# Kernel optimization log

Measured on AMD Instinct MI355X. Metric: run time of the kernel, lower is better.

The kernel has to match this reference:

```python
import jax, jax.numpy as jnp
import numpy as np

NEG_INF = -jnp.inf

def setup_inputs() -> dict:
    key = jax.random.key(0)
    k1, k2, k3, k4, k5 = jax.random.split(key, 5)
    b, n, d = 8, 1024, 2048
    s = 1.0 / np.sqrt(d)  # keep activations well-scaled (kaiming-ish)
    return {
        "y":  jax.random.normal(k1, (b, n, d), dtype=jnp.float32),
        "Wk": jax.random.normal(k2, (d, d), dtype=jnp.float32) * s,
        "Wq": jax.random.normal(k3, (d, d), dtype=jnp.float32) * s,
        "Wv": jax.random.normal(k4, (d, d), dtype=jnp.float32) * s,
        "Wo": jax.random.normal(k5, (d, d), dtype=jnp.float32) * s,
    }

def reference(y, Wk, Wq, Wv, Wo):
    # nn.Linear(bias=False): x @ W.T
    K = jnp.einsum('bnd,ed->bne', y, Wk)
    Q = 0.1 * jnp.einsum('bnd,ed->bne', y, Wq)
    V = jnp.einsum('bnd,ed->bne', y, Wv)
    # logits[b,i,j] = Q_i . K_j
    logits = jnp.einsum('bid,bjd->bij', Q, K)
    n = y.shape[1]
    diag = jnp.eye(n, dtype=bool)  # self-exclusion mask on the diagonal
    logits = jnp.where(diag[None, :, :], NEG_INF, logits)
    # NOTE: softmax over dim=1 (rows of the score matrix), non-standard axis
    attention_weights = jax.nn.softmax(logits, axis=1)
    # dropout(p=0.5) treated as identity (eval/deterministic reference)
    # torch: (V^T @ W)^T  ==  out[b,i,:] = sum_j W[b,j,i] * V[b,j,:]
    out = jnp.einsum('bji,bjd->bid', attention_weights, V)
    out = jnp.einsum('bid,ed->bie', out, Wo)
    return (out, attention_weights)
```

## Files before the change

kernel.cpp:

```cpp
#include <hip/hip_runtime.h>

typedef unsigned short u16;
typedef __attribute__((ext_vector_type(8))) __bf16 bf16x8;
typedef __attribute__((ext_vector_type(4))) float f32x4;
typedef __attribute__((ext_vector_type(4))) unsigned short u16x4;
typedef __attribute__((ext_vector_type(8))) unsigned short u16x8;

#define GLOBAL_AS __attribute__((address_space(1)))
#define LDS_AS __attribute__((address_space(3)))

__device__ __forceinline__ void gload_lds16(const void* g, void* l) {
    __builtin_amdgcn_global_load_lds((const GLOBAL_AS void*)g, (LDS_AS void*)l, 16, 0, 0);
}

__device__ __forceinline__ u16 f2bf(float f) {
    union { float f; unsigned u; } x; x.f = f;
    unsigned r = x.u + 0x7FFFu + ((x.u >> 16) & 1u);
    return (u16)(r >> 16);
}
__device__ __forceinline__ float bf2f(u16 h) {
    union { unsigned u; float f; } x; x.u = ((unsigned)h) << 16;
    return x.f;
}
struct BfPair { u16 h, l; };
__device__ __forceinline__ BfPair split2(float v) {
    BfPair p;
    p.h = f2bf(v);
    p.l = f2bf(v - bf2f(p.h));
    return p;
}

#define TM 128
#define TN 128
#define BK 64

__global__ __launch_bounds__(256) void conv_bf(
    const float* __restrict__ src, u16* __restrict__ dst, int n8)
{
    const int stride = gridDim.x * 256;
    for (int i = blockIdx.x * 256 + threadIdx.x; i < n8; i += stride) {
        const float* g = src + (size_t)i * 8;
        f32x4 v0 = *(const f32x4*)g;
        f32x4 v1 = *(const f32x4*)(g + 4);
        u16x8 w;
        #pragma unroll
        for (int e = 0; e < 4; ++e) { w[e] = f2bf(v0[e]); w[e + 4] = f2bf(v1[e]); }
        *(u16x8*)(dst + (size_t)i * 8) = w;
    }
}

__global__ __launch_bounds__(256) void transpose3(
    const float* __restrict__ s0, const float* __restrict__ s1, const float* __restrict__ s2,
    u16* __restrict__ d0, u16* __restrict__ d1, u16* __restrict__ d2)
{
    __shared__ float tile[64][65];
    const int z = blockIdx.z;
    const float* S = (z == 0) ? s0 : (z == 1) ? s1 : s2;
    u16* D = (z == 0) ? d0 : (z == 1) ? d1 : d2;
    const int x0 = blockIdx.x * 64;
    const int y0 = blockIdx.y * 64;
    const int t = threadIdx.x;
    const int rt = t >> 4;
    const int c4 = (t & 15) * 4;

    #pragma unroll
    for (int p = 0; p < 4; ++p) {
        const int r = p * 16 + rt;
        f32x4 v = *(const f32x4*)(S + (size_t)(y0 + r) * 2048 + x0 + c4);
        #pragma unroll
        for (int e = 0; e < 4; ++e) tile[r][c4 + e] = v[e];
    }
    __syncthreads();
    #pragma unroll
    for (int p = 0; p < 4; ++p) {
        const int a = p * 16 + rt;
        u16x4 w;
        #pragma unroll
        for (int e = 0; e < 4; ++e) w[e] = f2bf(tile[c4 + e][a]);
        *(u16x4*)(D + (size_t)(x0 + a) * 2048 + y0 + c4) = w;
    }
}

__global__ __launch_bounds__(256, 2) void gemm_pre(
    const u16* __restrict__ A0, const u16* __restrict__ B0,
    u16* __restrict__ GH, u16* __restrict__ GL, float alpha0,
    const u16* __restrict__ A1, const u16* __restrict__ B1, u16* __restrict__ U1,
    int N, int K)
{
    __shared__ u16 As0[TM * BK];
    __shared__ u16 Bs0[TN * BK];
    __shared__ u16 As1[TM * BK];
    __shared__ u16 Bs1[TN * BK];

    const int n0 = blockIdx.x * TN;
    const int m0 = blockIdx.y * TM;
    const int tid = threadIdx.x;
    const int lane = tid & 63;
    const int wave = tid >> 6;
    const int wm = (wave >> 1) * 64;
    const int wn = (wave & 1) * 64;
    const int quad = lane >> 4;
    const int lrow = lane & 15;

    f32x4 acc0[4][4] = {};
    f32x4 acc1[4][4] = {};

    for (int k0 = 0; k0 < K; k0 += BK) {
        #pragma unroll
        for (int r = 0; r < 4; ++r) {
            const int wbase = r * 4096 + wave * 1024;
            const int o = wbase + lane * 16;
            const int row = o >> 7;
            const int ce = (o & 127) >> 1;
            const size_t ao = (size_t)(m0 + row) * K + k0 + ce;
            const size_t bo = (size_t)(n0 + row) * K + k0 + ce;
            gload_lds16(A0 + ao, (char*)As0 + wbase);
            gload_lds16(B0 + bo, (char*)Bs0 + wbase);
            gload_lds16(A1 + ao, (char*)As1 + wbase);
            gload_lds16(B1 + bo, (char*)Bs1 + wbase);
        }
        __syncthreads();

        #pragma unroll
        for (int kk = 0; kk < BK; kk += 32) {
            bf16x8 a0[4], b0[4], a1[4], b1[4];
            #pragma unroll
            for (int t = 0; t < 4; ++t) {
                const int ra = (wm + t * 16 + lrow) * BK + kk + quad * 8;
                const int rb = (wn + t * 16 + lrow) * BK + kk + quad * 8;
                a0[t] = *(const bf16x8*)&As0[ra];
                b0[t] = *(const bf16x8*)&Bs0[rb];
                a1[t] = *(const bf16x8*)&As1[ra];
                b1[t] = *(const bf16x8*)&Bs1[rb];
            }
            #pragma unroll
            for (int ti = 0; ti < 4; ++ti)
                #pragma unroll
                for (int tj = 0; tj < 4; ++tj) {
                    acc0[ti][tj] = __builtin_amdgcn_mfma_f32_16x16x32_bf16(
                        a0[ti], b0[tj], acc0[ti][tj], 0, 0, 0);
                    acc1[ti][tj] = __builtin_amdgcn_mfma_f32_16x16x32_bf16(
                        a1[ti], b1[tj], acc1[ti][tj], 0, 0, 0);
                }
        }
        __syncthreads();
    }

    #pragma unroll
    for (int ti = 0; ti < 4; ++ti)
        #pragma unroll
        for (int tj = 0; tj < 4; ++tj) {
            const int nn = n0 + wn + tj * 16 + lrow;
            #pragma unroll
            for (int r2 = 0; r2 < 4; ++r2) {
                const int mm = m0 + wm + ti * 16 + quad * 4 + r2;
                BfPair p = split2(acc0[ti][tj][r2] * alpha0);
                GH[(size_t)mm * N + nn] = p.h;
                GL[(size_t)mm * N + nn] = p.l;
                U1[(size_t)mm * N + nn] = f2bf(acc1[ti][tj][r2]);
            }
        }
}

template <bool OSPLIT>
__global__ __launch_bounds__(256) void gemm_bs(
    const u16* __restrict__ A,
    const u16* __restrict__ Bh, const u16* __restrict__ Bl,
    void* __restrict__ C, void* __restrict__ C2,
    int M, int N, int K, size_t sAb, size_t sBb, size_t sCb)
{
    __shared__ u16 As[TM * BK];
    __shared__ u16 Bsh[TN * BK];
    __shared__ u16 Bsl[TN * BK];

    const int z = blockIdx.z;
    const u16* Ab  = (const u16*)((const char*)A + (size_t)z * sAb);
    const u16* Bhb = (const u16*)((const char*)Bh + (size_t)z * sBb);
    const u16* Blb = (const u16*)((const char*)Bl + (size_t)z * sBb);

    const int n0 = blockIdx.x * TN;
    const int m0 = blockIdx.y * TM;
    const int tid = threadIdx.x;
    const int lane = tid & 63;
    const int wave = tid >> 6;
    const int wm = (wave >> 1) * 64;
    const int wn = (wave & 1) * 64;
    const int quad = lane >> 4;
    const int lrow = lane & 15;

    f32x4 acc[4][4] = {};

    for (int k0 = 0; k0 < K; k0 += BK) {
        #pragma unroll
        for (int r = 0; r < 4; ++r) {
            const int wbase = r * 4096 + wave * 1024;
            const int o = wbase + lane * 16;
            const int row = o >> 7;
            const int ce = (o & 127) >> 1;
            const size_t ao = (size_t)(m0 + row) * K + k0 + ce;
            const size_t bo = (size_t)(n0 + row) * K + k0 + ce;
            gload_lds16(Ab + ao, (char*)As + wbase);
            gload_lds16(Bhb + bo, (char*)Bsh + wbase);
            gload_lds16(Blb + bo, (char*)Bsl + wbase);
        }
        __syncthreads();

        #pragma unroll
        for (int kk = 0; kk < BK; kk += 32) {
            bf16x8 af[4], bh[4], bl[4];
            #pragma unroll
            for (int t = 0; t < 4; ++t) {
                const int ra = (wm + t * 16 + lrow) * BK + kk + quad * 8;
                const int rb = (wn + t * 16 + lrow) * BK + kk + quad * 8;
                af[t] = *(const bf16x8*)&As[ra];
                bh[t] = *(const bf16x8*)&Bsh[rb];
                bl[t] = *(const bf16x8*)&Bsl[rb];
            }
            #pragma unroll
            for (int ti = 0; ti < 4; ++ti)
                #pragma unroll
                for (int tj = 0; tj < 4; ++tj) {
                    acc[ti][tj] = __builtin_amdgcn_mfma_f32_16x16x32_bf16(
                        af[ti], bl[tj], acc[ti][tj], 0, 0, 0);
                    acc[ti][tj] = __builtin_amdgcn_mfma_f32_16x16x32_bf16(
                        af[ti], bh[tj], acc[ti][tj], 0, 0, 0);
                }
        }
        __syncthreads();
    }

    if (OSPLIT) {
        u16* Chb = (u16*)((char*)C + (size_t)z * sCb);
        u16* Clb = (u16*)((char*)C2 + (size_t)z * sCb);
        #pragma unroll
        for (int ti = 0; ti < 4; ++ti)
            #pragma unroll
            for (int tj = 0; tj < 4; ++tj) {
                const int nn = n0 + wn + tj * 16 + lrow;
                #pragma unroll
                for (int r2 = 0; r2 < 4; ++r2) {
                    const int mm = m0 + wm + ti * 16 + quad * 4 + r2;
                    BfPair p = split2(acc[ti][tj][r2]);
                    Chb[(size_t)mm * N + nn] = p.h;
                    Clb[(size_t)mm * N + nn] = p.l;
                }
            }
    } else {
        float* Cb = (float*)((char*)C + (size_t)z * sCb);
        #pragma unroll
        for (int ti = 0; ti < 4; ++ti)
            #pragma unroll
            for (int tj = 0; tj < 4; ++tj) {
                const int nn = n0 + wn + tj * 16 + lrow;
                #pragma unroll
                for (int r2 = 0; r2 < 4; ++r2) {
                    const int mm = m0 + wm + ti * 16 + quad * 4 + r2;
                    Cb[(size_t)mm * N + nn] = acc[ti][tj][r2];
                }
            }
    }
}

__global__ __launch_bounds__(256, 2) void gemm_vo(
    const u16* __restrict__ A, const u16* __restrict__ B,
    u16* __restrict__ C,
    int M, int N, int K, size_t sBb, size_t sCb)
{
    __shared__ u16 As[TM * BK];
    __shared__ u16 Bs0[TN * BK];
    __shared__ u16 Bs1[TN * BK];

    const int z0 = blockIdx.z * 2;
    const u16* B0b = (const u16*)((const char*)B + (size_t)z0 * sBb);
    const u16* B1b = (const u16*)((const char*)B + (size_t)(z0 + 1) * sBb);

    const int n0 = blockIdx.x * TN;
    const int m0 = blockIdx.y * TM;
    const int tid = threadIdx.x;
    const int lane = tid & 63;
    const int wave = tid >> 6;
    const int wm = (wave >> 1) * 64;
    const int wn = (wave & 1) * 64;
    const int quad = lane >> 4;
    const int lrow = lane & 15;

    f32x4 acc0[4][4] = {};
    f32x4 acc1[4][4] = {};

    for (int k0 = 0; k0 < K; k0 += BK) {
        #pragma unroll
        for (int r = 0; r < 4; ++r) {
            const int wbase = r * 4096 + wave * 1024;
            const int o = wbase + lane * 16;
            const int row = o >> 7;
            const int ce = (o & 127) >> 1;
            const size_t ao = (size_t)(m0 + row) * K + k0 + ce;
            const size_t bo = (size_t)(n0 + row) * K + k0 + ce;
            gload_lds16(A + ao, (char*)As + wbase);
            gload_lds16(B0b + bo, (char*)Bs0 + wbase);
            gload_lds16(B1b + bo, (char*)Bs1 + wbase);
        }
        __syncthreads();

        #pragma unroll
        for (int kk = 0; kk < BK; kk += 32) {
            bf16x8 af[4], b0[4], b1[4];
            #pragma unroll
            for (int t = 0; t < 4; ++t) {
                const int ra = (wm + t * 16 + lrow) * BK + kk + quad * 8;
                const int rb = (wn + t * 16 + lrow) * BK + kk + quad * 8;
                af[t] = *(const bf16x8*)&As[ra];
                b0[t] = *(const bf16x8*)&Bs0[rb];
                b1[t] = *(const bf16x8*)&Bs1[rb];
            }
            #pragma unroll
            for (int ti = 0; ti < 4; ++ti)
                #pragma unroll
                for (int tj = 0; tj < 4; ++tj) {
                    acc0[ti][tj] = __builtin_amdgcn_mfma_f32_16x16x32_bf16(
                        af[ti], b0[tj], acc0[ti][tj], 0, 0, 0);
                    acc1[ti][tj] = __builtin_amdgcn_mfma_f32_16x16x32_bf16(
                        af[ti], b1[tj], acc1[ti][tj], 0, 0, 0);
                }
        }
        __syncthreads();
    }

    u16* C0 = (u16*)((char*)C + (size_t)z0 * sCb);
    u16* C1 = (u16*)((char*)C + (size_t)(z0 + 1) * sCb);
    #pragma unroll
    for (int ti = 0; ti < 4; ++ti)
        #pragma unroll
        for (int tj = 0; tj < 4; ++tj) {
            const int nn = n0 + wn + tj * 16 + lrow;
            #pragma unroll
            for (int r2 = 0; r2 < 4; ++r2) {
                const int mm = m0 + wm + ti * 16 + quad * 4 + r2;
                C0[(size_t)mm * N + nn] = f2bf(acc0[ti][tj][r2]);
                C1[(size_t)mm * N + nn] = f2bf(acc1[ti][tj][r2]);
            }
        }
}

__global__ __launch_bounds__(256) void gemm_fin(
    const u16* __restrict__ Ah, const u16* __restrict__ Al,
    const u16* __restrict__ B, float* __restrict__ C,
    int M, int N, int K, size_t sAb, size_t sBb, size_t sCb)
{
    __shared__ u16 Ash[TM * BK];
    __shared__ u16 Asl[TM * BK];
    __shared__ u16 Bs[TN * BK];

    const int z = blockIdx.z;
    const u16* Ahb = (const u16*)((const char*)Ah + (size_t)z * sAb);
    const u16* Alb = (const u16*)((const char*)Al + (size_t)z * sAb);
    const u16* Bb  = (const u16*)((const char*)B + (size_t)z * sBb);

    const int n0 = blockIdx.x * TN;
    const int m0 = blockIdx.y * TM;
    const int tid = threadIdx.x;
    const int lane = tid & 63;
    const int wave = tid >> 6;
    const int wm = (wave >> 1) * 64;
    const int wn = (wave & 1) * 64;
    const int quad = lane >> 4;
    const int lrow = lane & 15;

    f32x4 acc[4][4] = {};

    for (int k0 = 0; k0 < K; k0 += BK) {
        #pragma unroll
        for (int r = 0; r < 4; ++r) {
            const int wbase = r * 4096 + wave * 1024;
            const int o = wbase + lane * 16;
            const int row = o >> 7;
            const int ce = (o & 127) >> 1;
            const size_t ao = (size_t)(m0 + row) * K + k0 + ce;
            const size_t bo = (size_t)(n0 + row) * K + k0 + ce;
            gload_lds16(Ahb + ao, (char*)Ash + wbase);
            gload_lds16(Alb + ao, (char*)Asl + wbase);
            gload_lds16(Bb + bo, (char*)Bs + wbase);
        }
        __syncthreads();

        #pragma unroll
        for (int kk = 0; kk < BK; kk += 32) {
            bf16x8 ah[4], al[4], bfr[4];
            #pragma unroll
            for (int t = 0; t < 4; ++t) {
                const int ra = (wm + t * 16 + lrow) * BK + kk + quad * 8;
                ah[t] = *(const bf16x8*)&Ash[ra];
                al[t] = *(const bf16x8*)&Asl[ra];
                bfr[t] = *(const bf16x8*)&Bs[(wn + t * 16 + lrow) * BK + kk + quad * 8];
            }
            #pragma unroll
            for (int ti = 0; ti < 4; ++ti)
                #pragma unroll
                for (int tj = 0; tj < 4; ++tj) {
                    acc[ti][tj] = __builtin_amdgcn_mfma_f32_16x16x32_bf16(
                        al[ti], bfr[tj], acc[ti][tj], 0, 0, 0);
                    acc[ti][tj] = __builtin_amdgcn_mfma_f32_16x16x32_bf16(
                        ah[ti], bfr[tj], acc[ti][tj], 0, 0, 0);
                }
        }
        __syncthreads();
    }

    float* Cb = (float*)((char*)C + (size_t)z * sCb);
    #pragma unroll
    for (int ti = 0; ti < 4; ++ti)
        #pragma unroll
        for (int tj = 0; tj < 4; ++tj) {
            const int nn = n0 + wn + tj * 16 + lrow;
            #pragma unroll
            for (int r2 = 0; r2 < 4; ++r2) {
                const int mm = m0 + wm + ti * 16 + quad * 4 + r2;
                Cb[(size_t)mm * N + nn] = acc[ti][tj][r2];
            }
        }
}

__global__ __launch_bounds__(256) void softmax_split(
    const float* __restrict__ Lh, u16* __restrict__ Th, u16* __restrict__ Tl)
{
    const int lane = threadIdx.x & 63;
    const int wave = threadIdx.x >> 6;
    const size_t row = (size_t)blockIdx.x * 4 + wave;
    const int i = (int)(row & 1023);
    const float* src = Lh + row * 1024;
    const float NEG = -__builtin_inff();

    float v[16];
    float mx = NEG;
    #pragma unroll
    for (int cc = 0; cc < 4; ++cc) {
        f32x4 x = *(const f32x4*)(src + cc * 256 + lane * 4);
        #pragma unroll
        for (int e = 0; e < 4; ++e) {
            const int j = cc * 256 + lane * 4 + e;
            const float val = (j == i) ? NEG : x[e];
            v[cc * 4 + e] = val;
            mx = fmaxf(mx, val);
        }
    }
    #pragma unroll
    for (int off = 32; off > 0; off >>= 1) mx = fmaxf(mx, __shfl_xor(mx, off, 64));
    float s = 0.f;
    #pragma unroll
    for (int k = 0; k < 16; ++k) { v[k] = __expf(v[k] - mx); s += v[k]; }
    #pragma unroll
    for (int off = 32; off > 0; off >>= 1) s += __shfl_xor(s, off, 64);
    const float inv = 1.0f / s;

    #pragma unroll
    for (int cc = 0; cc < 4; ++cc) {
        u16x4 wh, wl;
        #pragma unroll
        for (int e = 0; e < 4; ++e) {
            BfPair p = split2(v[cc * 4 + e] * inv);
            wh[e] = p.h;
            wl[e] = p.l;
        }
        *(u16x4*)(Th + row * 1024 + cc * 256 + lane * 4) = wh;
        *(u16x4*)(Tl + row * 1024 + cc * 256 + lane * 4) = wl;
    }
}

__global__ __launch_bounds__(256) void transpose_attn_f32(
    const u16* __restrict__ Th, const u16* __restrict__ Tl, float* __restrict__ A)
{
    __shared__ float tile[64][65];
    const int bz = blockIdx.z;
    const int x0 = blockIdx.x * 64;
    const int y0 = blockIdx.y * 64;
    const size_t base = (size_t)bz * 1024 * 1024;
    float* dst = A + base;
    const int t = threadIdx.x;
    const int rt = t >> 4;
    const int c4 = (t & 15) * 4;

    #pragma unroll
    for (int p = 0; p < 4; ++p) {
        const int r = p * 16 + rt;
        const size_t off = base + (size_t)(y0 + r) * 1024 + x0 + c4;
        u16x4 vh = *(const u16x4*)(Th + off);
        u16x4 vl = *(const u16x4*)(Tl + off);
        #pragma unroll
        for (int e = 0; e < 4; ++e) tile[r][c4 + e] = bf2f(vh[e]) + bf2f(vl[e]);
    }
    __syncthreads();
    #pragma unroll
    for (int p = 0; p < 4; ++p) {
        const int a = p * 16 + rt;
        f32x4 w;
        #pragma unroll
        for (int e = 0; e < 4; ++e) w[e] = tile[c4 + e][a];
        *(f32x4*)(dst + (size_t)(x0 + a) * 1024 + y0 + c4) = w;
    }
}

extern "C" void kernel_launch(void* const* d_in, const int* in_sizes, int n_in,
                              void* d_out, int out_size, void* d_ws, size_t ws_size,
                              hipStream_t stream) {
    const float* y  = (const float*)d_in[0];
    const float* Wk = (const float*)d_in[1];
    const float* Wq = (const float*)d_in[2];
    const float* Wv = (const float*)d_in[3];
    const float* Wo = (const float*)d_in[4];

    const int b = 8, n = 1024, d = 2048;
    const int MB = b * n;
    const size_t MiB = 1024 * 1024;

    char* ws = (char*)d_ws;
    u16* yB  = (u16*)(ws);
    u16* WkT = (u16*)(ws + 32 * MiB);
    u16* WqT = (u16*)(ws + 40 * MiB);
    u16* WvT = (u16*)(ws + 48 * MiB);
    u16* WoB = (u16*)(ws + 56 * MiB);
    u16* GtH = (u16*)(ws + 64 * MiB);
    u16* GtL = (u16*)(ws + 72 * MiB);
    u16* UtB = (u16*)(ws + 80 * MiB);
    u16* ZcH = (u16*)(ws + 32 * MiB);
    u16* ZcL = (u16*)(ws + 88 * MiB);
    u16* Th  = (u16*)(ws + 32 * MiB);
    u16* Tl  = (u16*)(ws + 48 * MiB);
    u16* VOt = (u16*)(ws + 88 * MiB);

    float* outF = (float*)d_out;
    float* attF = outF + (size_t)MB * d;
    float* Lh   = (float*)d_out;

    dim3 blk(256);
    conv_bf<<<dim3(2048), blk, 0, stream>>>(y,  yB,  (MB * d) / 8);
    conv_bf<<<dim3(512),  blk, 0, stream>>>(Wo, WoB, (d * d) / 8);
    transpose3<<<dim3(32, 32, 3), blk, 0, stream>>>(Wk, Wq, Wv, WkT, WqT, WvT);
    gemm_pre<<<dim3(d / TN, d / TM, 1), blk, 0, stream>>>(
        WkT, WqT, GtH, GtL, 0.1f, WoB, WvT, UtB, d, d);
    gemm_bs<true><<<dim3(d / TN, MB / TM, 1), blk, 0, stream>>>(
        yB, GtH, GtL, ZcH, ZcL, MB, d, d, 0, 0, 0);
    gemm_bs<false><<<dim3(n / TN, n / TM, b), blk, 0, stream>>>(
        yB, ZcH, ZcL, Lh, nullptr, n, n, d,
        (size_t)n * d * 2, (size_t)n * d * 2, (size_t)n * n * 4);
    softmax_split<<<dim3(MB / 4), blk, 0, stream>>>(Lh, Th, Tl);
    transpose_attn_f32<<<dim3(16, 16, b), blk, 0, stream>>>(Th, Tl, attF);
    gemm_vo<<<dim3(n / TN, d / TM, b / 2), blk, 0, stream>>>(
        UtB, yB, VOt, d, n, d, (size_t)n * d * 2, (size_t)d * n * 2);
    gemm_fin<<<dim3(d / TN, n / TM, b), blk, 0, stream>>>(
        Th, Tl, VOt, outF, n, d, n,
        (size_t)n * n * 2, (size_t)d * n * 2, (size_t)n * d * 4);
}
```

Measured before the change: 643.8 us.

## Fuse logits and V·Wo GEMMs into one heterogeneous launch

Merges the batched logits GEMM (y·Zc split hi/lo) and the V·Wo GEMM into a single kernel whose first 512 blocks compute logits and remaining 1024 compute VOt, so both independent workloads fill the GPU together. It also drops the paired-batch register-heavy gemm_vo variant in favour of one batch per block. VOt is relocated into the output buffer's attention region, and the attention transpose is moved after gemm_fin so it runs once VOt is consumed. This removes one launch and a tail-effect gap, at the cost of a buffer-aliasing ordering dependency.

```diff
diff --git a/kernel.cpp b/kernel.cpp
--- a/kernel.cpp
+++ b/kernel.cpp
@@ -261,21 +261,15 @@
     }
 }
 
-__global__ __launch_bounds__(256, 2) void gemm_vo(
-    const u16* __restrict__ A, const u16* __restrict__ B,
-    u16* __restrict__ C,
-    int M, int N, int K, size_t sBb, size_t sCb)
-{
-    __shared__ u16 As[TM * BK];
-    __shared__ u16 Bs0[TN * BK];
-    __shared__ u16 Bs1[TN * BK];
-
-    const int z0 = blockIdx.z * 2;
-    const u16* B0b = (const u16*)((const char*)B + (size_t)z0 * sBb);
-    const u16* B1b = (const u16*)((const char*)B + (size_t)(z0 + 1) * sBb);
-
-    const int n0 = blockIdx.x * TN;
-    const int m0 = blockIdx.y * TM;
+__global__ __launch_bounds__(256) void gemm_lv(
+    const u16* __restrict__ yB, const u16* __restrict__ ZcH, const u16* __restrict__ ZcL,
+    float* __restrict__ Lh, const u16* __restrict__ Ut, u16* __restrict__ VOt)
+{
+    __shared__ u16 S0[TM * BK];
+    __shared__ u16 S1[TN * BK];
+    __shared__ u16 S2[TN * BK];
+
+    const int bid = blockIdx.x;
     const int tid = threadIdx.x;
     const int lane = tid & 63;
     const int wave = tid >> 6;
@@ -283,63 +277,115 @@
     const int wn = (wave & 1) * 64;
     const int quad = lane >> 4;
     const int lrow = lane & 15;
-
-    f32x4 acc0[4][4] = {};
-    f32x4 acc1[4][4] = {};
-
-    for (int k0 = 0; k0 < K; k0 += BK) {
-        #pragma unroll
-        for (int r = 0; r < 4; ++r) {
-            const int wbase = r * 4096 + wave * 1024;
-            const int o = wbase + lane * 16;
-            const int row = o >> 7;
-            const int ce = (o & 127) >> 1;
-            const size_t ao = (size_t)(m0 + row) * K + k0 + ce;
-            const size_t bo = (size_t)(n0 + row) * K + k0 + ce;
-            gload_lds16(A + ao, (char*)As + wbase);
-            gload_lds16(B0b + bo, (char*)Bs0 + wbase);
-            gload_lds16(B1b + bo, (char*)Bs1 + wbase);
-        }
-        __syncthreads();
-
-        #pragma unroll
-        for (int kk = 0; kk < BK; kk += 32) {
-            bf16x8 af[4], b0[4], b1[4];
-            #pragma unroll
-            for (int t = 0; t < 4; ++t) {
-                const int ra = (wm + t * 16 + lrow) * BK + kk + quad * 8;
-                const int rb = (wn + t * 16 + lrow) * BK + kk + quad * 8;
-                af[t] = *(const bf16x8*)&As[ra];
-                b0[t] = *(const bf16x8*)&Bs0[rb];
-                b1[t] = *(const bf16x8*)&Bs1[rb];
-            }
-            #pragma unroll
-            for (int ti = 0; ti < 4; ++ti)
-                #pragma unroll
-                for (int tj = 0; tj < 4; ++tj) {
-                    acc0[ti][tj] = __builtin_amdgcn_mfma_f32_16x16x32_bf16(
-                        af[ti], b0[tj], acc0[ti][tj], 0, 0, 0);
-                    acc1[ti][tj] = __builtin_amdgcn_mfma_f32_16x16x32_bf16(
-                        af[ti], b1[tj], acc1[ti][tj], 0, 0, 0);
-                }
-        }
-        __syncthreads();
-    }
-
-    u16* C0 = (u16*)((char*)C + (size_t)z0 * sCb);
-    u16* C1 = (u16*)((char*)C + (size_t)(z0 + 1) * sCb);
-    #pragma unroll
-    for (int ti = 0; ti < 4; ++ti)
-        #pragma unroll
-        for (int tj = 0; tj < 4; ++tj) {
-            const int nn = n0 + wn + tj * 16 + lrow;
-            #pragma unroll
-            for (int r2 = 0; r2 < 4; ++r2) {
-                const int mm = m0 + wm + ti * 16 + quad * 4 + r2;
-                C0[(size_t)mm * N + nn] = f2bf(acc0[ti][tj][r2]);
-                C1[(size_t)mm * N + nn] = f2bf(acc1[ti][tj][r2]);
-            }
-        }
+    const int K = 2048;
+
+    if (bid < 512) {
+        const int z = bid >> 6;
+        const int m0 = ((bid >> 3) & 7) * TM;
+        const int n0 = (bid & 7) * TN;
+        const u16* Ab  = yB  + (size_t)z * 1024 * 2048;
+        const u16* Bhb = ZcH + (size_t)z * 1024 * 2048;
+        const u16* Blb = ZcL + (size_t)z * 1024 * 2048;
+
+        f32x4 acc[4][4] = {};
+        for (int k0 = 0; k0 < K; k0 += BK) {
+            #pragma unroll
+            for (int r = 0; r < 4; ++r) {
+                const int wbase = r * 4096 + wave * 1024;
+                const int o = wbase + lane * 16;
+                const int row = o >> 7;
+                const int ce = (o & 127) >> 1;
+                const size_t ao = (size_t)(m0 + row) * K + k0 + ce;
+                const size_t bo = (size_t)(n0 + row) * K + k0 + ce;
+                gload_lds16(Ab + ao, (char*)S0 + wbase);
+                gload_lds16(Bhb + bo, (char*)S1 + wbase);
+                gload_lds16(Blb + bo, (char*)S2 + wbase);
+            }
+            __syncthreads();
+            #pragma unroll
+            for (int kk = 0; kk < BK; kk += 32) {
+                bf16x8 af[4], bh[4], bl[4];
+                #pragma unroll
+                for (int t = 0; t < 4; ++t) {
+                    const int ra = (wm + t * 16 + lrow) * BK + kk + quad * 8;
+                    const int rb = (wn + t * 16 + lrow) * BK + kk + quad * 8;
+                    af[t] = *(const bf16x8*)&S0[ra];
+                    bh[t] = *(const bf16x8*)&S1[rb];
+                    bl[t] = *(const bf16x8*)&S2[rb];
+                }
+                #pragma unroll
+                for (int ti = 0; ti < 4; ++ti)
+                    #pragma unroll
+                    for (int tj = 0; tj < 4; ++tj) {
+                        acc[ti][tj] = __builtin_amdgcn_mfma_f32_16x16x32_bf16(
+                            af[ti], bl[tj], acc[ti][tj], 0, 0, 0);
+                        acc[ti][tj] = __builtin_amdgcn_mfma_f32_16x16x32_bf16(
+                            af[ti], bh[tj], acc[ti][tj], 0, 0, 0);
+                    }
+            }
+            __syncthreads();
+        }
+        float* Cb = Lh + (size_t)z * 1024 * 1024;
+        #pragma unroll
+        for (int ti = 0; ti < 4; ++ti)
+            #pragma unroll
+            for (int tj = 0; tj < 4; ++tj) {
+                const int nn = n0 + wn + tj * 16 + lrow;
+                #pragma unroll
+                for (int r2 = 0; r2 < 4; ++r2) {
+                    const int mm = m0 + wm + ti * 16 + quad * 4 + r2;
+                    Cb[(size_t)mm * 1024 + nn] = acc[ti][tj][r2];
+                }
+            }
+    } else {
+        const int r0 = bid - 512;
+        const int z = r0 >> 7;
+        const int m0 = ((r0 >> 3) & 15) * TM;
+        const int n0 = (r0 & 7) * TN;
+        const u16* Bb = yB + (size_t)z * 1024 * 2048;
+
+        f32x4 acc[4][4] = {};
+        for (int k0 = 0; k0 < K; k0 += BK) {
+            #pragma unroll
+            for (int r = 0; r < 4; ++r) {
+                const int wbase = r * 4096 + wave * 1024;
+                const int o = wbase + lane * 16;
+                const int row = o >> 7;
+                const int ce = (o & 127) >> 1;
+                gload_lds16(Ut + (size_t)(m0 + row) * K + k0 + ce, (char*)S0 + wbase);
+                gload_lds16(Bb + (size_t)(n0 + row) * K + k0 + ce, (char*)S1 + wbase);
+            }
+            __syncthreads();
+            #pragma unroll
+            for (int kk = 0; kk < BK; kk += 32) {
+                bf16x8 af[4], bfr[4];
+                #pragma unroll
+                for (int t = 0; t < 4; ++t) {
+                    af[t]  = *(const bf16x8*)&S0[(wm + t * 16 + lrow) * BK + kk + quad * 8];
+                    bfr[t] = *(const bf16x8*)&S1[(wn + t * 16 + lrow) * BK + kk + quad * 8];
+                }
+                #pragma unroll
+                for (int ti = 0; ti < 4; ++ti)
+                    #pragma unroll
+                    for (int tj = 0; tj < 4; ++tj)
+                        acc[ti][tj] = __builtin_amdgcn_mfma_f32_16x16x32_bf16(
+                            af[ti], bfr[tj], acc[ti][tj], 0, 0, 0);
+            }
+            __syncthreads();
+        }
+        u16* Cb = VOt + (size_t)z * 2048 * 1024;
+        #pragma unroll
+        for (int ti = 0; ti < 4; ++ti)
+            #pragma unroll
+            for (int tj = 0; tj < 4; ++tj) {
+                const int nn = n0 + wn + tj * 16 + lrow;
+                #pragma unroll
+                for (int r2 = 0; r2 < 4; ++r2) {
+                    const int mm = m0 + wm + ti * 16 + quad * 4 + r2;
+                    Cb[(size_t)mm * 1024 + nn] = f2bf(acc[ti][tj][r2]);
+                }
+            }
+    }
 }
 
 __global__ __launch_bounds__(256) void gemm_fin(
@@ -525,11 +571,11 @@
     u16* ZcL = (u16*)(ws + 88 * MiB);
     u16* Th  = (u16*)(ws + 32 * MiB);
     u16* Tl  = (u16*)(ws + 48 * MiB);
-    u16* VOt = (u16*)(ws + 88 * MiB);
 
     float* outF = (float*)d_out;
     float* attF = outF + (size_t)MB * d;
     float* Lh   = (float*)d_out;
+    u16*   VOt  = (u16*)((char*)d_out + 64 * MiB);
 
     dim3 blk(256);
     conv_bf<<<dim3(2048), blk, 0, stream>>>(y,  yB,  (MB * d) / 8);
@@ -539,14 +585,10 @@
         WkT, WqT, GtH, GtL, 0.1f, WoB, WvT, UtB, d, d);
     gemm_bs<true><<<dim3(d / TN, MB / TM, 1), blk, 0, stream>>>(
         yB, GtH, GtL, ZcH, ZcL, MB, d, d, 0, 0, 0);
-    gemm_bs<false><<<dim3(n / TN, n / TM, b), blk, 0, stream>>>(
-        yB, ZcH, ZcL, Lh, nullptr, n, n, d,
-        (size_t)n * d * 2, (size_t)n * d * 2, (size_t)n * n * 4);
+    gemm_lv<<<dim3(1536), blk, 0, stream>>>(yB, ZcH, ZcL, Lh, UtB, VOt);
     softmax_split<<<dim3(MB / 4), blk, 0, stream>>>(Lh, Th, Tl);
-    transpose_attn_f32<<<dim3(16, 16, b), blk, 0, stream>>>(Th, Tl, attF);
-    gemm_vo<<<dim3(n / TN, d / TM, b / 2), blk, 0, stream>>>(
-        UtB, yB, VOt, d, n, d, (size_t)n * d * 2, (size_t)d * n * 2);
     gemm_fin<<<dim3(d / TN, n / TM, b), blk, 0, stream>>>(
         Th, Tl, VOt, outF, n, d, n,
         (size_t)n * n * 2, (size_t)d * n * 2, (size_t)n * d * 4);
-}
+    transpose_attn_f32<<<dim3(16, 16, b), blk, 0, stream>>>(Th, Tl, attF);
+}
```

Measured after the change: 657.8 us. 1.02x slower.
